# Kernel tuning notes

Measured on AMD Instinct MI355X. Metric: run time of the kernel, lower is better.

The kernel has to match this reference:

```python
import jax, jax.numpy as jnp
import numpy as np

N_BONDS = 50000
N_EDGES = 600000
BOND_DIM = 64
SPH_DIM = 64
UNITS = 64


def setup_inputs() -> dict:
    key = jax.random.key(0)
    k1, k2, k3, k4, k5 = jax.random.split(key, 5)
    bond_features = jax.random.normal(k1, (N_BONDS, BOND_DIM), dtype=jnp.float32)
    edges_sph_features = jax.random.normal(k2, (N_EDGES, SPH_DIM), dtype=jnp.float32)
    # column 0: sorted segment ids (tf.math.segment_sum requires sorted ids)
    seg = jnp.sort(jax.random.randint(k3, (N_EDGES,), 0, N_BONDS, dtype=jnp.int32))
    nbr = jax.random.randint(k4, (N_EDGES,), 0, N_BONDS, dtype=jnp.int32)
    edges_neighbor = jnp.stack([seg, nbr], axis=1)  # [n_edges, 2]
    kernel = jax.random.normal(k5, (BOND_DIM + SPH_DIM, UNITS), dtype=jnp.float32) * 0.05
    bias = jnp.zeros((UNITS,), dtype=jnp.float32)
    return {
        "bond_features": bond_features,
        "edges_sph_features": edges_sph_features,
        "edges_neighbor": edges_neighbor,
        "kernel": kernel,
        "bias": bias,
    }


def reference(bond_features, edges_sph_features, edges_neighbor, kernel, bias):
    # gather bond features of the neighboring bond for each edge (line-graph)
    gathered = bond_features[edges_neighbor[:, 1]]            # [E, bond_dim]
    concated = jnp.concatenate([gathered, edges_sph_features], axis=-1)  # [E, bond_dim+sph_dim]
    # scatter-reduce into segments (sorted ids; fixed num_segments for jit)
    aggregated = jax.ops.segment_sum(
        concated, edges_neighbor[:, 0], num_segments=N_BONDS,
        indices_are_sorted=True,
    )  # [n_bonds, bond_dim+sph_dim]
    return aggregated @ kernel + bias
```

## Files before the change

### kernel.cpp

```cpp
#include <hip/hip_runtime.h>

#define N_BONDS 50000
#define N_EDGES 600000
#define R_BONDS 4
#define THREADS 512
#define BONDS_PER_BLOCK 32

typedef float f4 __attribute__((ext_vector_type(4)));

__device__ __forceinline__ float bcastf(float v, int l) {
    return __builtin_bit_cast(float, __builtin_amdgcn_readlane(__builtin_bit_cast(int, v), l));
}
__device__ __forceinline__ f4 f4zero() { return (f4){0.f, 0.f, 0.f, 0.f}; }
__device__ __forceinline__ void fma4(f4& a, float s, const f4& b) {
    a.x = fmaf(s, b.x, a.x); a.y = fmaf(s, b.y, a.y);
    a.z = fmaf(s, b.z, a.z); a.w = fmaf(s, b.w, a.w);
}

__global__ __launch_bounds__(256)
void fill_starts(const int* __restrict__ edges, int* __restrict__ starts) {
    const int e = blockIdx.x * blockDim.x + threadIdx.x;
    if (e >= N_EDGES) return;
    const int2* edges2 = (const int2*)edges;
    const int s  = edges2[e].x;
    const int sp = (e == 0) ? -1 : edges2[e - 1].x;
    for (int b = sp + 1; b <= s; ++b) starts[b] = e;
    if (e == N_EDGES - 1)
        for (int b = s + 1; b <= N_BONDS; ++b) starts[b] = N_EDGES;
}

__global__ __launch_bounds__(THREADS, 4)
void fused_gather_segsum_mm(const float* __restrict__ bond,
                            const float* __restrict__ sph,
                            const int*   __restrict__ edges,
                            const float* __restrict__ Kmat,
                            const float* __restrict__ bias,
                            const int*   __restrict__ starts,
                            float* __restrict__ out)
{
    __shared__ float ldsK[128 * 64];
    const int tid  = threadIdx.x;
    const int lane = tid & 63;
    const int wid  = tid >> 6;
    const int fl   = lane & 15;
    const int sg   = lane >> 4;

    {
        const f4* K4 = (const f4*)Kmat;
        f4*       L4 = (f4*)ldsK;
        #pragma unroll
        for (int i = 0; i < 4; ++i) L4[tid + i * THREADS] = K4[tid + i * THREADS];
    }
    __syncthreads();

    const int b0 = blockIdx.x * BONDS_PER_BLOCK + wid * R_BONDS;
    if (b0 >= N_BONDS) return;

    int st[R_BONDS + 1];
    #pragma unroll
    for (int r = 0; r <= R_BONDS; ++r)
        st[r] = __builtin_amdgcn_readfirstlane(starts[b0 + r]);

    const int eb    = st[0];
    const int total = st[R_BONDS] - eb;
    const int nq    = (total + 3) >> 2;

    const f4* bond4 = (const f4*)bond;
    const f4* sph4  = (const f4*)sph;

    float slotG[R_BONDS], slotS[R_BONDS];
    f4 aG = f4zero(), aS = f4zero();
    int r = 0, cs = 0, bnd = st[1] - eb;

    auto txr = [&](f4 v) -> float {
        v.x += __shfl_xor(v.x, 16); v.y += __shfl_xor(v.y, 16);
        v.z += __shfl_xor(v.z, 16); v.w += __shfl_xor(v.w, 16);
        v.x += __shfl_xor(v.x, 32); v.y += __shfl_xor(v.y, 32);
        v.z += __shfl_xor(v.z, 32); v.w += __shfl_xor(v.w, 32);
        const int src = lane >> 2;
        const float s0 = __shfl(v.x, src), s1 = __shfl(v.y, src);
        const float s2 = __shfl(v.z, src), s3 = __shfl(v.w, src);
        const float r01 = (lane & 1) ? s1 : s0;
        const float r23 = (lane & 1) ? s3 : s2;
        return (lane & 2) ? r23 : r01;
    };

    auto slowpath = [&](int q, f4 GV, f4 SV) {
        const int qe = q + sg;
        while (true) {
            const float m = (qe >= cs && qe < bnd) ? 1.f : 0.f;
            fma4(aG, m, GV); fma4(aS, m, SV);
            if (bnd > q + 4) break;
            const float tG = txr(aG), tS = txr(aS);
            #pragma unroll
            for (int rr = 0; rr < R_BONDS; ++rr)
                if (rr == r) { slotG[rr] = tG; slotS[rr] = tS; }
            aG = f4zero(); aS = f4zero();
            cs = bnd;
            ++r;
            if (r >= R_BONDS) { bnd = 0x7fffffff; break; }
            #pragma unroll
            for (int rr = 2; rr <= R_BONDS; ++rr)
                if (r + 1 == rr) bnd = st[rr] - eb;
        }
    };

    auto loadIdx = [&](int Q) -> int {
        if (Q >= nq) return 0;
        int e = 4 * Q + sg;
        e = (e < total) ? e : total - 1;
        return edges[2 * (eb + e) + 1];
    };
    auto issData = [&](int nbr, int Q, f4& GV, f4& SV) {
        int e = 4 * Q + sg;
        e = (e < total) ? e : total - 1;
        GV = bond4[nbr * 16 + fl];
        SV = sph4[(eb + e) * 16 + fl];
    };
    auto accq = [&](int Q, f4 GV, f4 SV) {
        const int q_ = Q * 4;
        if (q_ + 4 <= bnd) { aG += GV; aS += SV; }
        else slowpath(q_, GV, SV);
    };

    if (nq > 0) {
        f4 gA = f4zero(), sA = f4zero(), gB = f4zero(), sB = f4zero();
        f4 gC = f4zero(), sC = f4zero(), gD = f4zero(), sD = f4zero();

        int i0 = loadIdx(0), i1 = loadIdx(1), i2 = loadIdx(2), i3 = loadIdx(3);
        int j0 = loadIdx(4), j1 = loadIdx(5), j2 = loadIdx(6), j3 = loadIdx(7);

        issData(i0, 0, gA, sA);
        if (1 < nq) issData(i1, 1, gB, sB);
        if (2 < nq) issData(i2, 2, gC, sC);
        if (3 < nq) issData(i3, 3, gD, sD);
        i0 = j0; i1 = j1; i2 = j2; i3 = j3;
        j0 = loadIdx(8); j1 = loadIdx(9); j2 = loadIdx(10); j3 = loadIdx(11);

        for (int q = 0; q < nq; q += 4) {
            accq(q + 0, gA, sA);
            if (q + 4 < nq) issData(i0, q + 4, gA, sA);
            if (q + 1 < nq) { accq(q + 1, gB, sB); if (q + 5 < nq) issData(i1, q + 5, gB, sB); }
            if (q + 2 < nq) { accq(q + 2, gC, sC); if (q + 6 < nq) issData(i2, q + 6, gC, sC); }
            if (q + 3 < nq) { accq(q + 3, gD, sD); if (q + 7 < nq) issData(i3, q + 7, gD, sD); }
            i0 = j0; i1 = j1; i2 = j2; i3 = j3;
            j0 = loadIdx(q + 12); j1 = loadIdx(q + 13);
            j2 = loadIdx(q + 14); j3 = loadIdx(q + 15);
        }
    }

    {
        const float tG = txr(aG), tS = txr(aS);
        #pragma unroll
        for (int rr = 0; rr < R_BONDS; ++rr) {
            if (rr == r)     { slotG[rr] = tG;  slotS[rr] = tS; }
            else if (rr > r) { slotG[rr] = 0.f; slotS[rr] = 0.f; }
        }
    }

    float acc[R_BONDS];
    const float bl = bias[lane];
    #pragma unroll
    for (int rr = 0; rr < R_BONDS; ++rr) acc[rr] = bl;

    #pragma unroll 4
    for (int d = 0; d < 64; ++d) {
        const float kt = ldsK[d * 64 + lane];
        const float kb = ldsK[(64 + d) * 64 + lane];
        #pragma unroll
        for (int rr = 0; rr < R_BONDS; ++rr) {
            acc[rr] = fmaf(bcastf(slotG[rr], d), kt, acc[rr]);
            acc[rr] = fmaf(bcastf(slotS[rr], d), kb, acc[rr]);
        }
    }

    #pragma unroll
    for (int rr = 0; rr < R_BONDS; ++rr)
        if (b0 + rr < N_BONDS)
            __builtin_nontemporal_store(acc[rr], &out[(b0 + rr) * 64 + lane]);
}

extern "C" void kernel_launch(void* const* d_in, const int* in_sizes, int n_in,
                              void* d_out, int out_size, void* d_ws, size_t ws_size,
                              hipStream_t stream) {
    const float* bond  = (const float*)d_in[0];
    const float* sph   = (const float*)d_in[1];
    const int*   edges = (const int*)d_in[2];
    const float* Kmat  = (const float*)d_in[3];
    const float* bias  = (const float*)d_in[4];
    float* out  = (float*)d_out;
    int* starts = (int*)d_ws;

    fill_starts<<<(N_EDGES + 255) / 256, 256, 0, stream>>>(edges, starts);

    const int nblocks = (N_BONDS + BONDS_PER_BLOCK - 1) / BONDS_PER_BLOCK;
    fused_gather_segsum_mm<<<nblocks, THREADS, 0, stream>>>(bond, sph, edges, Kmat,
                                                            bias, starts, out);
}
```

Baseline: 72.74 us.

## Batch sph and gathered bond loads in groups of eight with separate accumulation streams

Replaces the rolling four-deep software pipeline with an eight-quad batch: all sph loads are issued first, then all gathered bond loads, with sched barriers between the groups. The goal is more memory-level parallelism per wave. The G and S accumulators now run separate segment-boundary state machines so each stream can be consumed independently. Within a batch, loads are no longer overlapped with the previous batch's accumulation, and register pressure rises under the occupancy target of launch_bounds(512,4).

```diff
diff --git a/kernel.cpp b/kernel.cpp
--- a/kernel.cpp
+++ b/kernel.cpp
@@ -70,7 +70,8 @@
 
     float slotG[R_BONDS], slotS[R_BONDS];
     f4 aG = f4zero(), aS = f4zero();
-    int r = 0, cs = 0, bnd = st[1] - eb;
+    int rS = 0, csS = 0, bndS = st[1] - eb;
+    int rG = 0, csG = 0, bndG = st[1] - eb;
 
     auto txr = [&](f4 v) -> float {
         v.x += __shfl_xor(v.x, 16); v.y += __shfl_xor(v.y, 16);
@@ -85,24 +86,47 @@
         return (lane & 2) ? r23 : r01;
     };
 
-    auto slowpath = [&](int q, f4 GV, f4 SV) {
+    auto slowS = [&](int q, f4 XV) {
         const int qe = q + sg;
         while (true) {
-            const float m = (qe >= cs && qe < bnd) ? 1.f : 0.f;
-            fma4(aG, m, GV); fma4(aS, m, SV);
-            if (bnd > q + 4) break;
-            const float tG = txr(aG), tS = txr(aS);
-            #pragma unroll
-            for (int rr = 0; rr < R_BONDS; ++rr)
-                if (rr == r) { slotG[rr] = tG; slotS[rr] = tS; }
-            aG = f4zero(); aS = f4zero();
-            cs = bnd;
-            ++r;
-            if (r >= R_BONDS) { bnd = 0x7fffffff; break; }
-            #pragma unroll
-            for (int rr = 2; rr <= R_BONDS; ++rr)
-                if (r + 1 == rr) bnd = st[rr] - eb;
-        }
+            const float m = (qe >= csS && qe < bndS) ? 1.f : 0.f;
+            fma4(aS, m, XV);
+            if (bndS > q + 4) break;
+            const float tX = txr(aS);
+            #pragma unroll
+            for (int rr = 0; rr < R_BONDS; ++rr) if (rr == rS) slotS[rr] = tX;
+            aS = f4zero();
+            csS = bndS;
+            ++rS;
+            if (rS >= R_BONDS) { bndS = 0x7fffffff; break; }
+            #pragma unroll
+            for (int rr = 2; rr <= R_BONDS; ++rr) if (rS + 1 == rr) bndS = st[rr] - eb;
+        }
+    };
+    auto accS = [&](int Q, f4 XV) {
+        const int q_ = Q * 4;
+        if (q_ + 4 <= bndS) aS += XV; else slowS(q_, XV);
+    };
+    auto slowG = [&](int q, f4 XV) {
+        const int qe = q + sg;
+        while (true) {
+            const float m = (qe >= csG && qe < bndG) ? 1.f : 0.f;
+            fma4(aG, m, XV);
+            if (bndG > q + 4) break;
+            const float tX = txr(aG);
+            #pragma unroll
+            for (int rr = 0; rr < R_BONDS; ++rr) if (rr == rG) slotG[rr] = tX;
+            aG = f4zero();
+            csG = bndG;
+            ++rG;
+            if (rG >= R_BONDS) { bndG = 0x7fffffff; break; }
+            #pragma unroll
+            for (int rr = 2; rr <= R_BONDS; ++rr) if (rG + 1 == rr) bndG = st[rr] - eb;
+        }
+    };
+    auto accG = [&](int Q, f4 XV) {
+        const int q_ = Q * 4;
+        if (q_ + 4 <= bndG) aG += XV; else slowG(q_, XV);
     };
 
     auto loadIdx = [&](int Q) -> int {
@@ -111,50 +135,82 @@
         e = (e < total) ? e : total - 1;
         return edges[2 * (eb + e) + 1];
     };
-    auto issData = [&](int nbr, int Q, f4& GV, f4& SV) {
+    auto loadSph = [&](int Q) -> f4 {
         int e = 4 * Q + sg;
         e = (e < total) ? e : total - 1;
-        GV = bond4[nbr * 16 + fl];
-        SV = sph4[(eb + e) * 16 + fl];
-    };
-    auto accq = [&](int Q, f4 GV, f4 SV) {
-        const int q_ = Q * 4;
-        if (q_ + 4 <= bnd) { aG += GV; aS += SV; }
-        else slowpath(q_, GV, SV);
-    };
+        return sph4[(eb + e) * 16 + fl];
+    };
+
+    f4 v0, v1, v2, v3, v4, v5, v6, v7;
+    f4 g0, g1, g2, g3, g4, g5, g6, g7;
+    int ia0, ia1, ia2, ia3, ia4, ia5, ia6, ia7;
+    int ib0, ib1, ib2, ib3, ib4, ib5, ib6, ib7;
 
     if (nq > 0) {
-        f4 gA = f4zero(), sA = f4zero(), gB = f4zero(), sB = f4zero();
-        f4 gC = f4zero(), sC = f4zero(), gD = f4zero(), sD = f4zero();
-
-        int i0 = loadIdx(0), i1 = loadIdx(1), i2 = loadIdx(2), i3 = loadIdx(3);
-        int j0 = loadIdx(4), j1 = loadIdx(5), j2 = loadIdx(6), j3 = loadIdx(7);
-
-        issData(i0, 0, gA, sA);
-        if (1 < nq) issData(i1, 1, gB, sB);
-        if (2 < nq) issData(i2, 2, gC, sC);
-        if (3 < nq) issData(i3, 3, gD, sD);
-        i0 = j0; i1 = j1; i2 = j2; i3 = j3;
-        j0 = loadIdx(8); j1 = loadIdx(9); j2 = loadIdx(10); j3 = loadIdx(11);
-
-        for (int q = 0; q < nq; q += 4) {
-            accq(q + 0, gA, sA);
-            if (q + 4 < nq) issData(i0, q + 4, gA, sA);
-            if (q + 1 < nq) { accq(q + 1, gB, sB); if (q + 5 < nq) issData(i1, q + 5, gB, sB); }
-            if (q + 2 < nq) { accq(q + 2, gC, sC); if (q + 6 < nq) issData(i2, q + 6, gC, sC); }
-            if (q + 3 < nq) { accq(q + 3, gD, sD); if (q + 7 < nq) issData(i3, q + 7, gD, sD); }
-            i0 = j0; i1 = j1; i2 = j2; i3 = j3;
-            j0 = loadIdx(q + 12); j1 = loadIdx(q + 13);
-            j2 = loadIdx(q + 14); j3 = loadIdx(q + 15);
+        ia0 = loadIdx(0); ia1 = loadIdx(1); ia2 = loadIdx(2); ia3 = loadIdx(3);
+        ia4 = loadIdx(4); ia5 = loadIdx(5); ia6 = loadIdx(6); ia7 = loadIdx(7);
+
+        for (int Q0 = 0; Q0 < nq; Q0 += 8) {
+            ib0 = loadIdx(Q0 + 8);  ib1 = loadIdx(Q0 + 9);
+            ib2 = loadIdx(Q0 + 10); ib3 = loadIdx(Q0 + 11);
+            ib4 = loadIdx(Q0 + 12); ib5 = loadIdx(Q0 + 13);
+            ib6 = loadIdx(Q0 + 14); ib7 = loadIdx(Q0 + 15);
+
+            v0 = loadSph(Q0 + 0);
+            v1 = (Q0 + 1 < nq) ? loadSph(Q0 + 1) : f4zero();
+            v2 = (Q0 + 2 < nq) ? loadSph(Q0 + 2) : f4zero();
+            v3 = (Q0 + 3 < nq) ? loadSph(Q0 + 3) : f4zero();
+            v4 = (Q0 + 4 < nq) ? loadSph(Q0 + 4) : f4zero();
+            v5 = (Q0 + 5 < nq) ? loadSph(Q0 + 5) : f4zero();
+            v6 = (Q0 + 6 < nq) ? loadSph(Q0 + 6) : f4zero();
+            v7 = (Q0 + 7 < nq) ? loadSph(Q0 + 7) : f4zero();
+            __builtin_amdgcn_sched_barrier(0);
+
+            g0 = bond4[ia0 * 16 + fl];
+            g1 = (Q0 + 1 < nq) ? bond4[ia1 * 16 + fl] : f4zero();
+            g2 = (Q0 + 2 < nq) ? bond4[ia2 * 16 + fl] : f4zero();
+            g3 = (Q0 + 3 < nq) ? bond4[ia3 * 16 + fl] : f4zero();
+            g4 = (Q0 + 4 < nq) ? bond4[ia4 * 16 + fl] : f4zero();
+            g5 = (Q0 + 5 < nq) ? bond4[ia5 * 16 + fl] : f4zero();
+            g6 = (Q0 + 6 < nq) ? bond4[ia6 * 16 + fl] : f4zero();
+            g7 = (Q0 + 7 < nq) ? bond4[ia7 * 16 + fl] : f4zero();
+            __builtin_amdgcn_sched_barrier(0);
+
+            accS(Q0 + 0, v0);
+            if (Q0 + 1 < nq) accS(Q0 + 1, v1);
+            if (Q0 + 2 < nq) accS(Q0 + 2, v2);
+            if (Q0 + 3 < nq) accS(Q0 + 3, v3);
+            if (Q0 + 4 < nq) accS(Q0 + 4, v4);
+            if (Q0 + 5 < nq) accS(Q0 + 5, v5);
+            if (Q0 + 6 < nq) accS(Q0 + 6, v6);
+            if (Q0 + 7 < nq) accS(Q0 + 7, v7);
+
+            accG(Q0 + 0, g0);
+            if (Q0 + 1 < nq) accG(Q0 + 1, g1);
+            if (Q0 + 2 < nq) accG(Q0 + 2, g2);
+            if (Q0 + 3 < nq) accG(Q0 + 3, g3);
+            if (Q0 + 4 < nq) accG(Q0 + 4, g4);
+            if (Q0 + 5 < nq) accG(Q0 + 5, g5);
+            if (Q0 + 6 < nq) accG(Q0 + 6, g6);
+            if (Q0 + 7 < nq) accG(Q0 + 7, g7);
+
+            ia0 = ib0; ia1 = ib1; ia2 = ib2; ia3 = ib3;
+            ia4 = ib4; ia5 = ib5; ia6 = ib6; ia7 = ib7;
         }
     }
 
     {
-        const float tG = txr(aG), tS = txr(aS);
+        const float tS_ = txr(aS);
         #pragma unroll
         for (int rr = 0; rr < R_BONDS; ++rr) {
-            if (rr == r)     { slotG[rr] = tG;  slotS[rr] = tS; }
-            else if (rr > r) { slotG[rr] = 0.f; slotS[rr] = 0.f; }
+            if (rr == rS)     slotS[rr] = tS_;
+            else if (rr > rS) slotS[rr] = 0.f;
+        }
+        const float tG_ = txr(aG);
+        #pragma unroll
+        for (int rr = 0; rr < R_BONDS; ++rr) {
+            if (rr == rG)     slotG[rr] = tG_;
+            else if (rr > rG) slotG[rr] = 0.f;
         }
     }
 
```

Result: slower. 82.50 us (+13.4%).

## Split waves into gather and stream roles with LDS handoff before matmul

Applied to the files above, without the earlier changes.

Each block's 8 waves are split into two roles. Four waves gather neighbor bond features, and four waves stream the contiguous sph features, each covering 8 bonds. The partial sums go through LDS, and after a block barrier every wave does the matmul for 4 bonds. The aim is to let the latency-bound random gathers and the bandwidth-bound streaming loads run in separate waves, and to drop the register-heavy dual accumulators. The cost is extra LDS use, an extra barrier, and a double-length serial segment walk per wave.

```diff
diff --git a/kernel.cpp b/kernel.cpp
--- a/kernel.cpp
+++ b/kernel.cpp
@@ -2,9 +2,9 @@
 
 #define N_BONDS 50000
 #define N_EDGES 600000
-#define R_BONDS 4
 #define THREADS 512
 #define BONDS_PER_BLOCK 32
+#define GB 8
 
 typedef float f4 __attribute__((ext_vector_type(4)));
 
@@ -30,15 +30,18 @@
 }
 
 __global__ __launch_bounds__(THREADS, 4)
-void fused_gather_segsum_mm(const float* __restrict__ bond,
-                            const float* __restrict__ sph,
-                            const int*   __restrict__ edges,
-                            const float* __restrict__ Kmat,
-                            const float* __restrict__ bias,
-                            const int*   __restrict__ starts,
-                            float* __restrict__ out)
+void fused_wavesplit(const float* __restrict__ bond,
+                     const float* __restrict__ sph,
+                     const int*   __restrict__ edges,
+                     const float* __restrict__ Kmat,
+                     const float* __restrict__ bias,
+                     const int*   __restrict__ starts,
+                     float* __restrict__ out)
 {
     __shared__ float ldsK[128 * 64];
+    __shared__ float ldsG[BONDS_PER_BLOCK * 64];
+    __shared__ float ldsS[BONDS_PER_BLOCK * 64];
+
     const int tid  = threadIdx.x;
     const int lane = tid & 63;
     const int wid  = tid >> 6;
@@ -51,25 +54,23 @@
         #pragma unroll
         for (int i = 0; i < 4; ++i) L4[tid + i * THREADS] = K4[tid + i * THREADS];
     }
-    __syncthreads();
-
-    const int b0 = blockIdx.x * BONDS_PER_BLOCK + wid * R_BONDS;
-    if (b0 >= N_BONDS) return;
-
-    int st[R_BONDS + 1];
+
+    const bool isStream = (wid >= 4);
+    const int  grp = wid & 3;
+    const int  b0  = blockIdx.x * BONDS_PER_BLOCK + grp * GB;
+
+    int st[GB + 1];
     #pragma unroll
-    for (int r = 0; r <= R_BONDS; ++r)
-        st[r] = __builtin_amdgcn_readfirstlane(starts[b0 + r]);
-
+    for (int r = 0; r <= GB; ++r) {
+        int ix = b0 + r; if (ix > N_BONDS) ix = N_BONDS;
+        st[r] = __builtin_amdgcn_readfirstlane(starts[ix]);
+    }
     const int eb    = st[0];
-    const int total = st[R_BONDS] - eb;
+    const int total = st[GB] - eb;
     const int nq    = (total + 3) >> 2;
 
-    const f4* bond4 = (const f4*)bond;
-    const f4* sph4  = (const f4*)sph;
-
-    float slotG[R_BONDS], slotS[R_BONDS];
-    f4 aG = f4zero(), aS = f4zero();
+    float slot[GB];
+    f4 aX = f4zero();
     int r = 0, cs = 0, bnd = st[1] - eb;
 
     auto txr = [&](f4 v) -> float {
@@ -85,99 +86,117 @@
         return (lane & 2) ? r23 : r01;
     };
 
-    auto slowpath = [&](int q, f4 GV, f4 SV) {
+    auto slowpath = [&](int q, f4 XV) {
         const int qe = q + sg;
         while (true) {
             const float m = (qe >= cs && qe < bnd) ? 1.f : 0.f;
-            fma4(aG, m, GV); fma4(aS, m, SV);
+            fma4(aX, m, XV);
             if (bnd > q + 4) break;
-            const float tG = txr(aG), tS = txr(aS);
+            const float tX = txr(aX);
             #pragma unroll
-            for (int rr = 0; rr < R_BONDS; ++rr)
-                if (rr == r) { slotG[rr] = tG; slotS[rr] = tS; }
-            aG = f4zero(); aS = f4zero();
+            for (int rr = 0; rr < GB; ++rr)
+                if (rr == r) slot[rr] = tX;
+            aX = f4zero();
             cs = bnd;
             ++r;
-            if (r >= R_BONDS) { bnd = 0x7fffffff; break; }
+            if (r >= GB) { bnd = 0x7fffffff; break; }
             #pragma unroll
-            for (int rr = 2; rr <= R_BONDS; ++rr)
+            for (int rr = 2; rr <= GB; ++rr)
                 if (r + 1 == rr) bnd = st[rr] - eb;
         }
     };
-
-    auto loadIdx = [&](int Q) -> int {
-        if (Q >= nq) return 0;
-        int e = 4 * Q + sg;
-        e = (e < total) ? e : total - 1;
-        return edges[2 * (eb + e) + 1];
+    auto accX = [&](int Q, f4 XV) {
+        const int q_ = Q * 4;
+        if (q_ + 4 <= bnd) aX += XV;
+        else slowpath(q_, XV);
     };
-    auto issData = [&](int nbr, int Q, f4& GV, f4& SV) {
-        int e = 4 * Q + sg;
-        e = (e < total) ? e : total - 1;
-        GV = bond4[nbr * 16 + fl];
-        SV = sph4[(eb + e) * 16 + fl];
-    };
-    auto accq = [&](int Q, f4 GV, f4 SV) {
-        const int q_ = Q * 4;
-        if (q_ + 4 <= bnd) { aG += GV; aS += SV; }
-        else slowpath(q_, GV, SV);
-    };
-
-    if (nq > 0) {
-        f4 gA = f4zero(), sA = f4zero(), gB = f4zero(), sB = f4zero();
-        f4 gC = f4zero(), sC = f4zero(), gD = f4zero(), sD = f4zero();
-
-        int i0 = loadIdx(0), i1 = loadIdx(1), i2 = loadIdx(2), i3 = loadIdx(3);
-        int j0 = loadIdx(4), j1 = loadIdx(5), j2 = loadIdx(6), j3 = loadIdx(7);
-
-        issData(i0, 0, gA, sA);
-        if (1 < nq) issData(i1, 1, gB, sB);
-        if (2 < nq) issData(i2, 2, gC, sC);
-        if (3 < nq) issData(i3, 3, gD, sD);
-        i0 = j0; i1 = j1; i2 = j2; i3 = j3;
-        j0 = loadIdx(8); j1 = loadIdx(9); j2 = loadIdx(10); j3 = loadIdx(11);
-
-        for (int q = 0; q < nq; q += 4) {
-            accq(q + 0, gA, sA);
-            if (q + 4 < nq) issData(i0, q + 4, gA, sA);
-            if (q + 1 < nq) { accq(q + 1, gB, sB); if (q + 5 < nq) issData(i1, q + 5, gB, sB); }
-            if (q + 2 < nq) { accq(q + 2, gC, sC); if (q + 6 < nq) issData(i2, q + 6, gC, sC); }
-            if (q + 3 < nq) { accq(q + 3, gD, sD); if (q + 7 < nq) issData(i3, q + 7, gD, sD); }
-            i0 = j0; i1 = j1; i2 = j2; i3 = j3;
-            j0 = loadIdx(q + 12); j1 = loadIdx(q + 13);
-            j2 = loadIdx(q + 14); j3 = loadIdx(q + 15);
+
+    if (!isStream) {
+        const f4* bond4 = (const f4*)bond;
+        auto loadIdx = [&](int Q) -> int {
+            if (Q >= nq) return 0;
+            int e = 4 * Q + sg;
+            e = (e < total) ? e : total - 1;
+            return edges[2 * (eb + e) + 1];
+        };
+        if (nq > 0) {
+            int ia0 = loadIdx(0), ia1 = loadIdx(1), ia2 = loadIdx(2), ia3 = loadIdx(3);
+            int ib0 = loadIdx(4), ib1 = loadIdx(5), ib2 = loadIdx(6), ib3 = loadIdx(7);
+            for (int Q = 0; Q < nq; Q += 4) {
+                f4 x0 = bond4[ia0 * 16 + fl];
+                f4 x1 = (Q + 1 < nq) ? bond4[ia1 * 16 + fl] : f4zero();
+                f4 x2 = (Q + 2 < nq) ? bond4[ia2 * 16 + fl] : f4zero();
+                f4 x3 = (Q + 3 < nq) ? bond4[ia3 * 16 + fl] : f4zero();
+                ia0 = ib0; ia1 = ib1; ia2 = ib2; ia3 = ib3;
+                ib0 = loadIdx(Q + 8);  ib1 = loadIdx(Q + 9);
+                ib2 = loadIdx(Q + 10); ib3 = loadIdx(Q + 11);
+                accX(Q + 0, x0);
+                if (Q + 1 < nq) accX(Q + 1, x1);
+                if (Q + 2 < nq) accX(Q + 2, x2);
+                if (Q + 3 < nq) accX(Q + 3, x3);
+            }
+        }
+    } else {
+        const f4* sph4 = (const f4*)sph;
+        for (int Q = 0; Q < nq; Q += 4) {
+            int e0 = 4 * Q + sg;              e0 = (e0 < total) ? e0 : total - 1;
+            int e1 = 4 * (Q + 1) + sg;        e1 = (e1 < total) ? e1 : total - 1;
+            int e2 = 4 * (Q + 2) + sg;        e2 = (e2 < total) ? e2 : total - 1;
+            int e3 = 4 * (Q + 3) + sg;        e3 = (e3 < total) ? e3 : total - 1;
+            f4 x0 = sph4[(eb + e0) * 16 + fl];
+            f4 x1 = (Q + 1 < nq) ? sph4[(eb + e1) * 16 + fl] : f4zero();
+            f4 x2 = (Q + 2 < nq) ? sph4[(eb + e2) * 16 + fl] : f4zero();
+            f4 x3 = (Q + 3 < nq) ? sph4[(eb + e3) * 16 + fl] : f4zero();
+            accX(Q + 0, x0);
+            if (Q + 1 < nq) accX(Q + 1, x1);
+            if (Q + 2 < nq) accX(Q + 2, x2);
+            if (Q + 3 < nq) accX(Q + 3, x3);
         }
     }
 
     {
-        const float tG = txr(aG), tS = txr(aS);
-        #pragma unroll
-        for (int rr = 0; rr < R_BONDS; ++rr) {
-            if (rr == r)     { slotG[rr] = tG;  slotS[rr] = tS; }
-            else if (rr > r) { slotG[rr] = 0.f; slotS[rr] = 0.f; }
-        }
-    }
-
-    float acc[R_BONDS];
+        const float tX = txr(aX);
+        #pragma unroll
+        for (int rr = 0; rr < GB; ++rr) {
+            if (rr == r)     slot[rr] = tX;
+            else if (rr > r) slot[rr] = 0.f;
+        }
+    }
+
+    {
+        float* dstL = isStream ? ldsS : ldsG;
+        #pragma unroll
+        for (int rr = 0; rr < GB; ++rr)
+            dstL[(grp * GB + rr) * 64 + lane] = slot[rr];
+    }
+    __syncthreads();
+
+    const int mb = wid * 4;
+    float vg[4], vs[4], acc[4];
     const float bl = bias[lane];
     #pragma unroll
-    for (int rr = 0; rr < R_BONDS; ++rr) acc[rr] = bl;
+    for (int rr = 0; rr < 4; ++rr) {
+        vg[rr] = ldsG[(mb + rr) * 64 + lane];
+        vs[rr] = ldsS[(mb + rr) * 64 + lane];
+        acc[rr] = bl;
+    }
 
     #pragma unroll 4
     for (int d = 0; d < 64; ++d) {
         const float kt = ldsK[d * 64 + lane];
         const float kb = ldsK[(64 + d) * 64 + lane];
         #pragma unroll
-        for (int rr = 0; rr < R_BONDS; ++rr) {
-            acc[rr] = fmaf(bcastf(slotG[rr], d), kt, acc[rr]);
-            acc[rr] = fmaf(bcastf(slotS[rr], d), kb, acc[rr]);
-        }
-    }
-
+        for (int rr = 0; rr < 4; ++rr) {
+            acc[rr] = fmaf(bcastf(vg[rr], d), kt, acc[rr]);
+            acc[rr] = fmaf(bcastf(vs[rr], d), kb, acc[rr]);
+        }
+    }
+
+    const int ob = blockIdx.x * BONDS_PER_BLOCK + mb;
     #pragma unroll
-    for (int rr = 0; rr < R_BONDS; ++rr)
-        if (b0 + rr < N_BONDS)
-            __builtin_nontemporal_store(acc[rr], &out[(b0 + rr) * 64 + lane]);
+    for (int rr = 0; rr < 4; ++rr)
+        if (ob + rr < N_BONDS)
+            __builtin_nontemporal_store(acc[rr], &out[(ob + rr) * 64 + lane]);
 }
 
 extern "C" void kernel_launch(void* const* d_in, const int* in_sizes, int n_in,
@@ -194,6 +213,6 @@
     fill_starts<<<(N_EDGES + 255) / 256, 256, 0, stream>>>(edges, starts);
 
     const int nblocks = (N_BONDS + BONDS_PER_BLOCK - 1) / BONDS_PER_BLOCK;
-    fused_gather_segsum_mm<<<nblocks, THREADS, 0, stream>>>(bond, sph, edges, Kmat,
-                                                            bias, starts, out);
-}
+    fused_wavesplit<<<nblocks, THREADS, 0, stream>>>(bond, sph, edges, Kmat,
+                                                     bias, starts, out);
+}
```

Measured after the change: 81.82 us. 12.5% more time.
